# Optimization experiments

Hardware: AMD Instinct MI355X
Metric: run time of the kernel (lower is better)

Reference implementation:

```python
import jax, jax.numpy as jnp
import numpy as np

VOCAB, BLOCK, D, H, E, TOPK = 50257, 2048, 1024, 8, 8, 2
HD = D // H  # head_size = 128


def _layernorm(x, g, b, eps=1e-5):
    mu = jnp.mean(x, axis=-1, keepdims=True)
    var = jnp.mean(jnp.square(x - mu), axis=-1, keepdims=True)
    return (x - mu) * jax.lax.rsqrt(var + eps) * g + b


def setup_inputs() -> dict:
    key = jax.random.key(0)
    ks = jax.random.split(key, 12)
    s = 0.02
    return {
        "idx": jax.random.randint(ks[0], (4, BLOCK), 0, VOCAB),
        "tok_table": jax.random.normal(ks[1], (VOCAB, D), jnp.float32) * s,
        "pos_table": jax.random.normal(ks[2], (BLOCK, D), jnp.float32) * s,
        "Wq": jax.random.normal(ks[3], (H, D, HD), jnp.float32) * s,
        "Wk": jax.random.normal(ks[4], (H, D, HD), jnp.float32) * s,
        "Wv": jax.random.normal(ks[5], (H, D, HD), jnp.float32) * s,
        "Wo": jax.random.normal(ks[6], (D, D), jnp.float32) * s,
        "bo": jnp.zeros((D,), jnp.float32),
        "g1": jnp.ones((D,), jnp.float32),
        "b1": jnp.zeros((D,), jnp.float32),
        "g2": jnp.ones((D,), jnp.float32),
        "b2": jnp.zeros((D,), jnp.float32),
        "Wr": jax.random.normal(ks[7], (D, E), jnp.float32) * s,
        "br": jnp.zeros((E,), jnp.float32),
        "Wn": jax.random.normal(ks[8], (D, E), jnp.float32) * s,
        "bn": jnp.zeros((E,), jnp.float32),
    }


def reference(idx, tok_table, pos_table, Wq, Wk, Wv, Wo, bo, g1, b1, g2, b2, Wr, br, Wn, bn):
    B, T = idx.shape
    x = tok_table[idx] + pos_table[:T]  # [B,T,D]

    # --- multi-head causal self-attention (dropout off / eval mode) ---
    xn = _layernorm(x, g1, b1)
    q = jnp.einsum('btc,hcd->bhtd', xn, Wq)
    k = jnp.einsum('btc,hcd->bhtd', xn, Wk)
    v = jnp.einsum('btc,hcd->bhtd', xn, Wv)
    # NOTE: original scales by C**-0.5 where C = n_embed (not head_size)
    wei = jnp.einsum('bhtd,bhsd->bhts', q, k) * (D ** -0.5)
    causal = jnp.tril(jnp.ones((T, T), bool))
    wei = jnp.where(causal, wei, -jnp.inf)
    wei = jax.nn.softmax(wei, axis=-1)
    attn = jnp.einsum('bhts,bhsd->bhtd', wei, v)  # [B,H,T,HD]
    attn = attn.transpose(0, 2, 1, 3).reshape(B, T, D)  # concat heads
    x = x + attn @ Wo + bo  # residual

    x_norm = _layernorm(x, g2, b2)

    # --- noisy top-k router ---
    logits = x_norm @ Wr + br          # [B,T,E]
    noise_logits = x_norm @ Wn + bn    # [B,T,E]
    noise = jax.random.normal(jax.random.key(42), logits.shape, logits.dtype)
    noisy = logits + noise * jax.nn.softplus(noise_logits)
    top_vals, indices = jax.lax.top_k(noisy, TOPK)  # [B,T,K]
    probs_k = jax.nn.softmax(top_vals, axis=-1)     # softmax over -inf-scattered logits == softmax over top-k
    router_probs = jnp.sum(jax.nn.one_hot(indices, E, dtype=probs_k.dtype) * probs_k[..., None], axis=-2)

    return (x_norm, router_probs, indices, x)
```

## Files before the change

kernel.cpp:

```cpp
#include <hip/hip_runtime.h>
#include <math.h>
#include <stdint.h>

typedef __attribute__((ext_vector_type(8))) _Float16 f16x8;
typedef __attribute__((ext_vector_type(4))) _Float16 f16x4;
typedef __attribute__((ext_vector_type(4))) float f32x4;

__device__ __forceinline__ void split_f16(float x, _Float16& h, _Float16& l) {
  h = (_Float16)x;
  l = (_Float16)((x - (float)h) * 2048.0f);
}

__device__ __forceinline__ void gld16(const void* g, void* l) {
  __builtin_amdgcn_global_load_lds(
      (const __attribute__((address_space(1))) void*)g,
      (__attribute__((address_space(3))) void*)l, 16, 0, 0);
}

__device__ __forceinline__ void threefry2x32_42(uint32_t x0, uint32_t x1,
                                                uint32_t& o0, uint32_t& o1) {
  const uint32_t k0 = 0u, k1 = 42u;
  const uint32_t k2 = k0 ^ k1 ^ 0x1BD11BDAu;
  x0 += k0; x1 += k1;
#define TF_R(r) { x0 += x1; x1 = (x1 << (r)) | (x1 >> (32 - (r))); x1 ^= x0; }
  TF_R(13) TF_R(15) TF_R(26) TF_R(6)
  x0 += k1; x1 += k2 + 1u;
  TF_R(17) TF_R(29) TF_R(16) TF_R(24)
  x0 += k2; x1 += k0 + 2u;
  TF_R(13) TF_R(15) TF_R(26) TF_R(6)
  x0 += k0; x1 += k1 + 3u;
  TF_R(17) TF_R(29) TF_R(16) TF_R(24)
  x0 += k1; x1 += k2 + 4u;
  TF_R(13) TF_R(15) TF_R(26) TF_R(6)
  x0 += k2; x1 += k0 + 5u;
#undef TF_R
  o0 = x0; o1 = x1;
}

__device__ __forceinline__ float jax_erfinv_f32(float x) {
  float xx = __fmul_rn(x, x);
  float w = -log1pf(-xx);
  float p;
  if (w < 5.0f) {
    w = __fadd_rn(w, -2.5f);
    p = 2.81022636e-08f;
    p = __fadd_rn(3.43273939e-07f, __fmul_rn(p, w));
    p = __fadd_rn(-3.5233877e-06f, __fmul_rn(p, w));
    p = __fadd_rn(-4.39150654e-06f, __fmul_rn(p, w));
    p = __fadd_rn(0.00021858087f, __fmul_rn(p, w));
    p = __fadd_rn(-0.00125372503f, __fmul_rn(p, w));
    p = __fadd_rn(-0.00417768164f, __fmul_rn(p, w));
    p = __fadd_rn(0.246640727f, __fmul_rn(p, w));
    p = __fadd_rn(1.50140941f, __fmul_rn(p, w));
  } else {
    w = __fadd_rn(sqrtf(w), -3.0f);
    p = -0.000200214257f;
    p = __fadd_rn(0.000100950558f, __fmul_rn(p, w));
    p = __fadd_rn(0.00134934322f, __fmul_rn(p, w));
    p = __fadd_rn(-0.00367342844f, __fmul_rn(p, w));
    p = __fadd_rn(0.00573950773f, __fmul_rn(p, w));
    p = __fadd_rn(-0.0076224613f, __fmul_rn(p, w));
    p = __fadd_rn(0.00943887047f, __fmul_rn(p, w));
    p = __fadd_rn(1.00167406f, __fmul_rn(p, w));
    p = __fadd_rn(2.83297682f, __fmul_rn(p, w));
  }
  return __fmul_rn(p, x);
}

__device__ __forceinline__ float jax_noise(uint32_t n) {
  uint32_t o0, o1;
  threefry2x32_42(0u, n, o0, o1);
  uint32_t bits = o0 ^ o1;
  uint32_t fb = (bits >> 9) | 0x3F800000u;
  float f = __fadd_rn(__uint_as_float(fb), -1.0f);
  const float lo = __uint_as_float(0xBF7FFFFFu);
  float u = __fadd_rn(__fmul_rn(f, 2.0f), lo);
  u = fmaxf(lo, u);
  return __fmul_rn(__uint_as_float(0x3FB504F3u), jax_erfinv_f32(u));
}

__device__ __forceinline__ float block_sum_256(float v, float* buf) {
  #pragma unroll
  for (int off = 32; off > 0; off >>= 1) v += __shfl_down(v, off, 64);
  int lane = threadIdx.x & 63;
  int w = threadIdx.x >> 6;
  if (lane == 0) buf[w] = v;
  __syncthreads();
  return buf[0] + buf[1] + buf[2] + buf[3];
}

__global__ __launch_bounds__(128) void k_wsplit(
    const float* __restrict__ Wq, const float* __restrict__ Wk,
    const float* __restrict__ Wv, const float* __restrict__ Wo,
    _Float16* __restrict__ wqt_h, _Float16* __restrict__ wqt_l,
    _Float16* __restrict__ wot_h, _Float16* __restrict__ wot_l) {
  int z = blockIdx.x, tid = threadIdx.x;
  const float* src;
  int ldn, n;
  _Float16 *dh, *dl;
  if (z < 24) {
    int which = z >> 3, h = z & 7;
    src = ((which == 0) ? Wq : (which == 1) ? Wk : Wv) + (size_t)h * 1024 * 128;
    ldn = 128; n = tid;
    dh = wqt_h + (size_t)z * 128 * 1024 + (size_t)n * 1024;
    dl = wqt_l + (size_t)z * 128 * 1024 + (size_t)n * 1024;
  } else {
    int zz = z - 24;
    src = Wo; ldn = 1024; n = zz * 128 + tid;
    dh = wot_h + (size_t)n * 1024;
    dl = wot_l + (size_t)n * 1024;
  }
  for (int k0 = 0; k0 < 1024; k0 += 16) {
    f16x8 hv0, hv1, lv0, lv1;
    #pragma unroll
    for (int j = 0; j < 8; ++j) {
      _Float16 hh, ll;
      split_f16(src[(size_t)(k0 + j) * ldn + n], hh, ll);
      hv0[j] = hh; lv0[j] = ll;
    }
    #pragma unroll
    for (int j = 0; j < 8; ++j) {
      _Float16 hh, ll;
      split_f16(src[(size_t)(k0 + 8 + j) * ldn + n], hh, ll);
      hv1[j] = hh; lv1[j] = ll;
    }
    *(f16x8*)(dh + k0) = hv0; *(f16x8*)(dh + k0 + 8) = hv1;
    *(f16x8*)(dl + k0) = lv0; *(f16x8*)(dl + k0 + 8) = lv1;
  }
}

__global__ __launch_bounds__(256) void k_embed_ln1(
    const int* __restrict__ idx, const float* __restrict__ tok,
    const float* __restrict__ pos, const float* __restrict__ g1,
    const float* __restrict__ b1, float* __restrict__ x_out,
    _Float16* __restrict__ xnh, _Float16* __restrict__ xnl) {
  __shared__ float bufA[4], bufB[4];
  int r = blockIdx.x;
  int t = r & 2047;
  int token = idx[r];
  int c4 = threadIdx.x;
  float4 tv = *((const float4*)(tok + (size_t)token * 1024) + c4);
  float4 pv = *((const float4*)(pos + (size_t)t * 1024) + c4);
  float4 xv = make_float4(tv.x + pv.x, tv.y + pv.y, tv.z + pv.z, tv.w + pv.w);
  *((float4*)(x_out + (size_t)r * 1024) + c4) = xv;
  float mu = block_sum_256(xv.x + xv.y + xv.z + xv.w, bufA) * (1.0f / 1024.0f);
  float d0 = xv.x - mu, d1 = xv.y - mu, d2 = xv.z - mu, d3 = xv.w - mu;
  float var = block_sum_256(d0*d0 + d1*d1 + d2*d2 + d3*d3, bufB) * (1.0f / 1024.0f);
  float rs = rsqrtf(var + 1e-5f);
  float4 gv = *((const float4*)g1 + c4);
  float4 bv = *((const float4*)b1 + c4);
  float xn0 = d0*rs*gv.x + bv.x, xn1 = d1*rs*gv.y + bv.y;
  float xn2 = d2*rs*gv.z + bv.z, xn3 = d3*rs*gv.w + bv.w;
  f16x4 hv, lv;
  _Float16 hh, ll;
  split_f16(xn0, hh, ll); hv[0] = hh; lv[0] = ll;
  split_f16(xn1, hh, ll); hv[1] = hh; lv[1] = ll;
  split_f16(xn2, hh, ll); hv[2] = hh; lv[2] = ll;
  split_f16(xn3, hh, ll); hv[3] = hh; lv[3] = ll;
  *(f16x4*)(xnh + (size_t)r * 1024 + c4 * 4) = hv;
  *(f16x4*)(xnl + (size_t)r * 1024 + c4 * 4) = lv;
}

__global__ __launch_bounds__(256) void k_ln2(
    const float* __restrict__ x, const float* __restrict__ g2,
    const float* __restrict__ b2, float* __restrict__ xn_out) {
  __shared__ float bufA[4], bufB[4];
  int r = blockIdx.x;
  int c4 = threadIdx.x;
  float4 xv = *((const float4*)(x + (size_t)r * 1024) + c4);
  float mu = block_sum_256(xv.x + xv.y + xv.z + xv.w, bufA) * (1.0f / 1024.0f);
  float d0 = xv.x - mu, d1 = xv.y - mu, d2 = xv.z - mu, d3 = xv.w - mu;
  float var = block_sum_256(d0*d0 + d1*d1 + d2*d2 + d3*d3, bufB) * (1.0f / 1024.0f);
  float rs = rsqrtf(var + 1e-5f);
  float4 gv = *((const float4*)g2 + c4);
  float4 bv = *((const float4*)b2 + c4);
  float4 xn = make_float4(d0*rs*gv.x + bv.x, d1*rs*gv.y + bv.y,
                          d2*rs*gv.z + bv.z, d3*rs*gv.w + bv.w);
  *((float4*)(xn_out + (size_t)r * 1024) + c4) = xn;
}

__global__ __launch_bounds__(256) void k_qkv(
    const _Float16* __restrict__ xnh, const _Float16* __restrict__ xnl,
    const _Float16* __restrict__ wth, const _Float16* __restrict__ wtl,
    _Float16* __restrict__ qh, _Float16* __restrict__ ql,
    _Float16* __restrict__ kh, _Float16* __restrict__ kl,
    _Float16* __restrict__ vth, _Float16* __restrict__ vtl) {
  __shared__ __align__(16) _Float16 Ah[128 * 32], Al[128 * 32];
  __shared__ __align__(16) _Float16 Bh[128 * 32], Bl[128 * 32];
  int z = blockIdx.x;
  int which = z >> 3, h = z & 7;
  int m0 = blockIdx.y * 128;
  int tid = threadIdx.x, w = tid >> 6, lane = tid & 63;
  const _Float16* bsh = wth + (size_t)z * 128 * 1024;
  const _Float16* bsl = wtl + (size_t)z * 128 * 1024;
  f32x4 om[2][8], oc[2][8];
  const f32x4 zero4 = {0.f, 0.f, 0.f, 0.f};
  #pragma unroll
  for (int mr = 0; mr < 2; ++mr)
    #pragma unroll
    for (int nb = 0; nb < 8; ++nb) { om[mr][nb] = zero4; oc[mr][nb] = zero4; }

  for (int k0 = 0; k0 < 1024; k0 += 32) {
    __syncthreads();
    #pragma unroll
    for (int i2 = 0; i2 < 2; ++i2) {
      int r = w * 32 + i2 * 16 + (lane >> 2);
      int gs = (lane & 3) ^ ((r >> 1) & 3);
      size_t ao = (size_t)(m0 + r) * 1024 + k0 + gs * 8;
      size_t bo_ = (size_t)r * 1024 + k0 + gs * 8;
      gld16(xnh + ao, &Ah[(w * 32 + i2 * 16) * 32]);
      gld16(xnl + ao, &Al[(w * 32 + i2 * 16) * 32]);
      gld16(bsh + bo_, &Bh[(w * 32 + i2 * 16) * 32]);
      gld16(bsl + bo_, &Bl[(w * 32 + i2 * 16) * 32]);
    }
    asm volatile("s_waitcnt vmcnt(0)" ::: "memory");
    __syncthreads();
    f16x8 ah[2], al[2];
    #pragma unroll
    for (int mr = 0; mr < 2; ++mr) {
      int arow = w * 32 + mr * 16 + (lane & 15);
      int ag = (lane >> 4) ^ ((arow >> 1) & 3);
      ah[mr] = *(f16x8*)&Ah[arow * 32 + ag * 8];
      al[mr] = *(f16x8*)&Al[arow * 32 + ag * 8];
    }
    #pragma unroll
    for (int nb = 0; nb < 8; ++nb) {
      int brow = nb * 16 + (lane & 15);
      int bg = (lane >> 4) ^ ((brow >> 1) & 3);
      f16x8 b8h = *(f16x8*)&Bh[brow * 32 + bg * 8];
      f16x8 b8l = *(f16x8*)&Bl[brow * 32 + bg * 8];
      #pragma unroll
      for (int mr = 0; mr < 2; ++mr) {
        om[mr][nb] = __builtin_amdgcn_mfma_f32_16x16x32_f16(ah[mr], b8h, om[mr][nb], 0, 0, 0);
        oc[mr][nb] = __builtin_amdgcn_mfma_f32_16x16x32_f16(ah[mr], b8l, oc[mr][nb], 0, 0, 0);
        oc[mr][nb] = __builtin_amdgcn_mfma_f32_16x16x32_f16(al[mr], b8h, oc[mr][nb], 0, 0, 0);
      }
    }
  }
  int bb = m0 >> 11, tb = m0 & 2047;
  if (which < 2) {
    _Float16* OH = (which == 0) ? qh : kh;
    _Float16* OL = (which == 0) ? ql : kl;
    size_t base = (size_t)(bb * 8 + h) * 2048 * 128;
    #pragma unroll
    for (int mr = 0; mr < 2; ++mr)
      #pragma unroll
      for (int r2 = 0; r2 < 4; ++r2) {
        int t = tb + w * 32 + mr * 16 + ((lane >> 4) << 2) + r2;
        size_t roff = base + (size_t)t * 128 + (lane & 15);
        #pragma unroll
        for (int nb = 0; nb < 8; ++nb) {
          float v = om[mr][nb][r2] + oc[mr][nb][r2] * (1.0f / 2048.0f);
          _Float16 hh, ll;
          split_f16(v, hh, ll);
          OH[roff + nb * 16] = hh;
          OL[roff + nb * 16] = ll;
        }
      }
  } else {
    size_t base = (size_t)(bb * 8 + h) * 128 * 2048;
    #pragma unroll
    for (int mr = 0; mr < 2; ++mr) {
      int t4 = tb + w * 32 + mr * 16 + ((lane >> 4) << 2);
      #pragma unroll
      for (int nb = 0; nb < 8; ++nb) {
        int col = nb * 16 + (lane & 15);
        size_t off = base + (size_t)col * 2048 + t4;
        f16x4 hv, lv;
        #pragma unroll
        for (int r2 = 0; r2 < 4; ++r2) {
          _Float16 hh, ll;
          split_f16(om[mr][nb][r2] + oc[mr][nb][r2] * (1.0f / 2048.0f), hh, ll);
          hv[r2] = hh; lv[r2] = ll;
        }
        *(f16x4*)(vth + off) = hv;
        *(f16x4*)(vtl + off) = lv;
      }
    }
  }
}

__global__ __launch_bounds__(256) void k_proj_res(
    const _Float16* __restrict__ ah_, const _Float16* __restrict__ al_,
    const _Float16* __restrict__ wth, const _Float16* __restrict__ wtl,
    const float* __restrict__ bo, float* __restrict__ x_io) {
  __shared__ __align__(16) _Float16 Ah[128 * 64], Al[128 * 64];
  __shared__ __align__(16) _Float16 Bh[128 * 64], Bl[128 * 64];
  int n0 = blockIdx.x * 128;
  int m0 = blockIdx.y * 128;
  int tid = threadIdx.x, w = tid >> 6, lane = tid & 63;
  f32x4 om[2][8], oc[2][8];
  const f32x4 zero4 = {0.f, 0.f, 0.f, 0.f};
  #pragma unroll
  for (int mr = 0; mr < 2; ++mr)
    #pragma unroll
    for (int nb = 0; nb < 8; ++nb) { om[mr][nb] = zero4; oc[mr][nb] = zero4; }

  for (int k0 = 0; k0 < 1024; k0 += 64) {
    __syncthreads();
    #pragma unroll
    for (int i2 = 0; i2 < 4; ++i2) {
      int r = w * 32 + i2 * 8 + (lane >> 3);
      int gs = (lane & 7) ^ (r & 7);
      size_t ao = (size_t)(m0 + r) * 1024 + k0 + gs * 8;
      size_t bo_ = (size_t)(n0 + r) * 1024 + k0 + gs * 8;
      gld16(ah_ + ao, &Ah[(w * 32 + i2 * 8) * 64]);
      gld16(al_ + ao, &Al[(w * 32 + i2 * 8) * 64]);
      gld16(wth + bo_, &Bh[(w * 32 + i2 * 8) * 64]);
      gld16(wtl + bo_, &Bl[(w * 32 + i2 * 8) * 64]);
    }
    asm volatile("s_waitcnt vmcnt(0)" ::: "memory");
    __syncthreads();
    #pragma unroll
    for (int k2 = 0; k2 < 2; ++k2) {
      f16x8 ah[2], al[2];
      #pragma unroll
      for (int mr = 0; mr < 2; ++mr) {
        int arow = w * 32 + mr * 16 + (lane & 15);
        int ag = (k2 * 4 + (lane >> 4)) ^ (arow & 7);
        ah[mr] = *(f16x8*)&Ah[arow * 64 + ag * 8];
        al[mr] = *(f16x8*)&Al[arow * 64 + ag * 8];
      }
      #pragma unroll
      for (int nb = 0; nb < 8; ++nb) {
        int brow = nb * 16 + (lane & 15);
        int bg = (k2 * 4 + (lane >> 4)) ^ (brow & 7);
        f16x8 b8h = *(f16x8*)&Bh[brow * 64 + bg * 8];
        f16x8 b8l = *(f16x8*)&Bl[brow * 64 + bg * 8];
        #pragma unroll
        for (int mr = 0; mr < 2; ++mr) {
          om[mr][nb] = __builtin_amdgcn_mfma_f32_16x16x32_f16(ah[mr], b8h, om[mr][nb], 0, 0, 0);
          oc[mr][nb] = __builtin_amdgcn_mfma_f32_16x16x32_f16(ah[mr], b8l, oc[mr][nb], 0, 0, 0);
          oc[mr][nb] = __builtin_amdgcn_mfma_f32_16x16x32_f16(al[mr], b8h, oc[mr][nb], 0, 0, 0);
        }
      }
    }
  }
  #pragma unroll
  for (int mr = 0; mr < 2; ++mr)
    #pragma unroll
    for (int nb = 0; nb < 8; ++nb) {
      int col = n0 + nb * 16 + (lane & 15);
      float bov = bo[col];
      #pragma unroll
      for (int r2 = 0; r2 < 4; ++r2) {
        int gm = m0 + w * 32 + mr * 16 + ((lane >> 4) << 2) + r2;
        float* p = x_io + (size_t)gm * 1024 + col;
        *p += om[mr][nb][r2] + oc[mr][nb][r2] * (1.0f / 2048.0f) + bov;
      }
    }
}

__global__ __launch_bounds__(512) void k_attn(
    const _Float16* __restrict__ qhp, const _Float16* __restrict__ qlp,
    const _Float16* __restrict__ khp, const _Float16* __restrict__ klp,
    const _Float16* __restrict__ vthp, const _Float16* __restrict__ vtlp,
    _Float16* __restrict__ attn_h, _Float16* __restrict__ attn_l) {
  __shared__ __align__(16) _Float16 Ksh[2][32 * 128];
  __shared__ __align__(16) _Float16 Ksl[2][32 * 128];
  __shared__ __align__(16) _Float16 Vh[2][128 * 32];
  __shared__ __align__(16) _Float16 Vl[2][128 * 32];
  __shared__ __align__(16) _Float16 Ph8[8][16 * 32];
  __shared__ __align__(16) _Float16 Pl8[8][16 * 32];

  int bh_ = blockIdx.x;
  int b = bh_ >> 3, h = bh_ & 7;
  int qs = blockIdx.y;
  int tid = threadIdx.x;
  int w = tid >> 6, lane = tid & 63;

  size_t bh = (size_t)(b * 8 + h) * 2048 * 128;
  const _Float16* qhb = qhp + bh;
  const _Float16* qlb = qlp + bh;
  const _Float16* khb = khp + bh;
  const _Float16* klb = klp + bh;
  const _Float16* vhb = vthp + bh;
  const _Float16* vlb = vtlp + bh;
  _Float16* Ph = &Ph8[w][0];
  _Float16* Pl = &Pl8[w][0];

  const f32x4 zero4 = {0.f, 0.f, 0.f, 0.f};

  auto stage = [&](int cur, int j0) {
    int kr = (w << 2) + (lane >> 4);
    int kg = (lane & 15) ^ (kr & 7);
    size_t kgo = (size_t)(j0 + kr) * 128 + kg * 8;
    gld16(khb + kgo, &Ksh[cur][(w << 2) * 128]);
    gld16(klb + kgo, &Ksl[cur][(w << 2) * 128]);
    int vr = (w << 4) + (lane >> 2);
    int vg = (lane & 3) ^ ((vr >> 1) & 3);
    size_t vgo = (size_t)vr * 2048 + j0 + vg * 8;
    gld16(vhb + vgo, &Vh[cur][(w << 4) * 32]);
    gld16(vlb + vgo, &Vl[cur][(w << 4) * 32]);
  };

  #pragma unroll 1
  for (int pi = 0; pi < 2; ++pi) {
    int qt = pi ? (15 - qs) : qs;
    int t0 = qt << 7;
    int tW = t0 + w * 16;
    int rowBase = tW + ((lane >> 4) << 2);

    size_t qoff = (size_t)(tW + (lane & 15)) * 128 + ((lane >> 4) << 3);
    f16x8 qfh[4], qfl[4];
    #pragma unroll
    for (int kk = 0; kk < 4; ++kk) {
      qfh[kk] = *(const f16x8*)(qhb + qoff + kk * 32);
      qfl[kk] = *(const f16x8*)(qlb + qoff + kk * 32);
    }

    f32x4 om[8], oc[8];
    #pragma unroll
    for (int db = 0; db < 8; ++db) { om[db] = zero4; oc[db] = zero4; }
    float mreg[4], lreg[4];
    #pragma unroll
    for (int r2 = 0; r2 < 4; ++r2) { mreg[r2] = -INFINITY; lreg[r2] = 0.f; }

    int nt = 4 * qt + 4;
    stage(0, 0);
    asm volatile("s_waitcnt vmcnt(0)" ::: "memory");
    __syncthreads();
    int cur = 0;

    #pragma unroll 1
    for (int t = 0; t < nt; ++t) {
      if (t + 1 < nt) stage(cur ^ 1, (t + 1) * 32);
      int j0 = t * 32;

      f32x4 sm[2], sc[2];
      #pragma unroll
      for (int nb = 0; nb < 2; ++nb) { sm[nb] = zero4; sc[nb] = zero4; }
      #pragma unroll
      for (int kk = 0; kk < 4; ++kk) {
        #pragma unroll
        for (int nb = 0; nb < 2; ++nb) {
          int krow = nb * 16 + (lane & 15);
          int kg = (kk * 4 + (lane >> 4)) ^ (krow & 7);
          f16x8 kfh = *(f16x8*)&Ksh[cur][krow * 128 + kg * 8];
          f16x8 kfl = *(f16x8*)&Ksl[cur][krow * 128 + kg * 8];
          sm[nb] = __builtin_amdgcn_mfma_f32_16x16x32_f16(qfh[kk], kfh, sm[nb], 0, 0, 0);
          sc[nb] = __builtin_amdgcn_mfma_f32_16x16x32_f16(qfh[kk], kfl, sc[nb], 0, 0, 0);
          sc[nb] = __builtin_amdgcn_mfma_f32_16x16x32_f16(qfl[kk], kfh, sc[nb], 0, 0, 0);
        }
      }

      float rmax[4];
      #pragma unroll
      for (int r2 = 0; r2 < 4; ++r2) rmax[r2] = -INFINITY;
      #pragma unroll
      for (int nb = 0; nb < 2; ++nb) {
        int col = j0 + nb * 16 + (lane & 15);
        #pragma unroll
        for (int r2 = 0; r2 < 4; ++r2) {
          float sv = (sm[nb][r2] + sc[nb][r2] * (1.0f / 2048.0f)) * 0.03125f;
          sv = (col > rowBase + r2) ? -INFINITY : sv;
          sm[nb][r2] = sv;
          rmax[r2] = fmaxf(rmax[r2], sv);
        }
      }
      #pragma unroll
      for (int mk = 1; mk < 16; mk <<= 1)
        #pragma unroll
        for (int r2 = 0; r2 < 4; ++r2)
          rmax[r2] = fmaxf(rmax[r2], __shfl_xor(rmax[r2], mk, 64));
      float alpha[4], rsum[4];
      bool newmax = false;
      #pragma unroll
      for (int r2 = 0; r2 < 4; ++r2) {
        float mnew = fmaxf(mreg[r2], rmax[r2]);
        newmax |= (mnew > mreg[r2]);
        alpha[r2] = __expf(mreg[r2] - mnew);
        mreg[r2] = mnew;
        rsum[r2] = 0.f;
      }
      #pragma unroll
      for (int nb = 0; nb < 2; ++nb)
        #pragma unroll
        for (int r2 = 0; r2 < 4; ++r2) {
          float p = __expf(sm[nb][r2] - mreg[r2]);
          sm[nb][r2] = p;
          rsum[r2] += p;
        }
      #pragma unroll
      for (int mk = 1; mk < 16; mk <<= 1)
        #pragma unroll
        for (int r2 = 0; r2 < 4; ++r2)
          rsum[r2] += __shfl_xor(rsum[r2], mk, 64);
      #pragma unroll
      for (int r2 = 0; r2 < 4; ++r2)
        lreg[r2] = lreg[r2] * alpha[r2] + rsum[r2];

      #pragma unroll
      for (int nb = 0; nb < 2; ++nb) {
        int col = nb * 16 + (lane & 15);
        #pragma unroll
        for (int r2 = 0; r2 < 4; ++r2) {
          int prow = ((lane >> 4) << 2) + r2;
          int sg = (col >> 3) ^ ((prow >> 1) & 3);
          float ps = sm[nb][r2] * 16384.0f;
          _Float16 hh, ll;
          split_f16(ps, hh, ll);
          Ph[prow * 32 + sg * 8 + (col & 7)] = hh;
          Pl[prow * 32 + sg * 8 + (col & 7)] = ll;
        }
      }

      if (__any((int)newmax)) {
        #pragma unroll
        for (int db = 0; db < 8; ++db)
          #pragma unroll
          for (int r2 = 0; r2 < 4; ++r2) {
            om[db][r2] *= alpha[r2];
            oc[db][r2] *= alpha[r2];
          }
      }

      {
        int prow = lane & 15;
        int pg = (lane >> 4) ^ ((prow >> 1) & 3);
        f16x8 pah = *(f16x8*)&Ph[prow * 32 + pg * 8];
        f16x8 pal = *(f16x8*)&Pl[prow * 32 + pg * 8];
        #pragma unroll
        for (int db = 0; db < 8; ++db) {
          int vrow = db * 16 + (lane & 15);
          int vg = (lane >> 4) ^ ((vrow >> 1) & 3);
          f16x8 vfh = *(f16x8*)&Vh[cur][vrow * 32 + vg * 8];
          f16x8 vfl = *(f16x8*)&Vl[cur][vrow * 32 + vg * 8];
          om[db] = __builtin_amdgcn_mfma_f32_16x16x32_f16(pah, vfh, om[db], 0, 0, 0);
          oc[db] = __builtin_amdgcn_mfma_f32_16x16x32_f16(pah, vfl, oc[db], 0, 0, 0);
          oc[db] = __builtin_amdgcn_mfma_f32_16x16x32_f16(pal, vfh, oc[db], 0, 0, 0);
        }
      }

      asm volatile("s_waitcnt vmcnt(0)" ::: "memory");
      __syncthreads();
      cur ^= 1;
    }

    size_t obase = ((size_t)(b * 2048 + rowBase)) * 1024 + h * 128 + (lane & 15);
    #pragma unroll
    for (int r2 = 0; r2 < 4; ++r2) {
      float inv = 1.f / (lreg[r2] * 16384.0f);
      #pragma unroll
      for (int db = 0; db < 8; ++db) {
        float v = (om[db][r2] + oc[db][r2] * (1.0f / 2048.0f)) * inv;
        _Float16 hh, ll;
        split_f16(v, hh, ll);
        attn_h[obase + (size_t)r2 * 1024 + db * 16] = hh;
        attn_l[obase + (size_t)r2 * 1024 + db * 16] = ll;
      }
    }
  }
}

__global__ __launch_bounds__(256) void k_router(
    const float* __restrict__ xn, const float* __restrict__ Wr,
    const float* __restrict__ br, const float* __restrict__ Wn,
    const float* __restrict__ bn, float* __restrict__ rp_out,
    float* __restrict__ idx_out) {
  int wave = threadIdx.x >> 6, lane = threadIdx.x & 63;
  int r = blockIdx.x * 4 + wave;
  const float* xr = xn + (size_t)r * 1024;
  float acc[16];
  #pragma unroll
  for (int i = 0; i < 16; ++i) acc[i] = 0.f;
  int cbase = lane * 16;
  for (int cc = 0; cc < 16; ++cc) {
    int c = cbase + cc;
    float xv = xr[c];
    const float4* wr4 = (const float4*)(Wr + (size_t)c * 8);
    float4 w0 = wr4[0], w1 = wr4[1];
    acc[0] += xv * w0.x; acc[1] += xv * w0.y; acc[2] += xv * w0.z; acc[3] += xv * w0.w;
    acc[4] += xv * w1.x; acc[5] += xv * w1.y; acc[6] += xv * w1.z; acc[7] += xv * w1.w;
    const float4* wn4 = (const float4*)(Wn + (size_t)c * 8);
    float4 n0 = wn4[0], n1 = wn4[1];
    acc[8]  += xv * n0.x; acc[9]  += xv * n0.y; acc[10] += xv * n0.z; acc[11] += xv * n0.w;
    acc[12] += xv * n1.x; acc[13] += xv * n1.y; acc[14] += xv * n1.z; acc[15] += xv * n1.w;
  }
  #pragma unroll
  for (int i = 0; i < 16; ++i) {
    #pragma unroll
    for (int off = 32; off > 0; off >>= 1) acc[i] += __shfl_down(acc[i], off, 64);
  }
  if (lane == 0) {
    float noisy[8];
    uint32_t nbase = (uint32_t)r * 8u;
    #pragma unroll
    for (int e = 0; e < 8; ++e) {
      float lg = acc[e] + br[e];
      float x = acc[8 + e] + bn[e];
      float sp = __fadd_rn(fmaxf(x, 0.f), log1pf(expf(-fabsf(x))));
      float nz = jax_noise(nbase + (uint32_t)e);
      noisy[e] = __fadd_rn(lg, __fmul_rn(nz, sp));
    }
    float v1 = -INFINITY, v2 = -INFINITY;
    int i1 = 0, i2 = 0;
    #pragma unroll
    for (int e = 0; e < 8; ++e) {
      float vv = noisy[e];
      if (vv > v1) { v2 = v1; i2 = i1; v1 = vv; i1 = e; }
      else if (vv > v2) { v2 = vv; i2 = e; }
    }
    float e2 = expf(v2 - v1);
    float ssum = 1.f + e2;
    float p1 = 1.f / ssum, p2 = e2 / ssum;
    float rp[8];
    #pragma unroll
    for (int e = 0; e < 8; ++e) rp[e] = 0.f;
    rp[i1] = p1; rp[i2] = p2;
    float* op = rp_out + (size_t)r * 8;
    #pragma unroll
    for (int e = 0; e < 8; ++e) op[e] = rp[e];
    idx_out[(size_t)r * 2]     = (float)i1;
    idx_out[(size_t)r * 2 + 1] = (float)i2;
  }
}

extern "C" void kernel_launch(void* const* d_in, const int* in_sizes, int n_in,
                              void* d_out, int out_size, void* d_ws, size_t ws_size,
                              hipStream_t stream) {
  const int*   idx = (const int*)d_in[0];
  const float* tok = (const float*)d_in[1];
  const float* pos = (const float*)d_in[2];
  const float* Wq  = (const float*)d_in[3];
  const float* Wk  = (const float*)d_in[4];
  const float* Wv  = (const float*)d_in[5];
  const float* Wo  = (const float*)d_in[6];
  const float* bo  = (const float*)d_in[7];
  const float* g1  = (const float*)d_in[8];
  const float* b1  = (const float*)d_in[9];
  const float* g2  = (const float*)d_in[10];
  const float* b2  = (const float*)d_in[11];
  const float* Wr  = (const float*)d_in[12];
  const float* br  = (const float*)d_in[13];
  const float* Wn  = (const float*)d_in[14];
  const float* bn  = (const float*)d_in[15];

  float* out_xnorm = (float*)d_out;
  float* out_rp    = out_xnorm + 8388608;
  float* out_idx   = out_rp + 65536;
  float* out_x     = out_idx + 16384;

  _Float16* xnh  = (_Float16*)d_ws;
  _Float16* xnl  = xnh + 8388608;
  _Float16* qhp  = xnl + 8388608;
  _Float16* qlp  = qhp + 8388608;
  _Float16* khp  = qlp + 8388608;
  _Float16* klp  = khp + 8388608;
  _Float16* vthp = klp + 8388608;
  _Float16* vtlp = vthp + 8388608;
  _Float16* attn_h = xnh;
  _Float16* attn_l = xnl;
  _Float16* wqt_h = (_Float16*)out_xnorm;
  _Float16* wqt_l = wqt_h + 3145728;
  _Float16* wot_h = wqt_l + 3145728;
  _Float16* wot_l = wot_h + 1048576;

  k_wsplit<<<32, 128, 0, stream>>>(Wq, Wk, Wv, Wo, wqt_h, wqt_l, wot_h, wot_l);
  k_embed_ln1<<<8192, 256, 0, stream>>>(idx, tok, pos, g1, b1, out_x, xnh, xnl);
  k_qkv<<<dim3(24, 64), 256, 0, stream>>>(xnh, xnl, wqt_h, wqt_l,
                                          qhp, qlp, khp, klp, vthp, vtlp);
  k_attn<<<dim3(32, 8), 512, 0, stream>>>(qhp, qlp, khp, klp, vthp, vtlp,
                                          attn_h, attn_l);
  k_proj_res<<<dim3(8, 64), 256, 0, stream>>>(attn_h, attn_l, wot_h, wot_l, bo, out_x);
  k_ln2<<<8192, 256, 0, stream>>>(out_x, g2, b2, out_xnorm);
  k_router<<<2048, 256, 0, stream>>>(out_xnorm, Wr, br, Wn, bn, out_rp, out_idx);
}
```

Measured before the change: 967.5 us.

## Double-buffer LDS tiles in QKV and output-projection GEMMs to overlap loads

Converts the QKV and output-projection GEMM main loops to a two-stage LDS pipeline. The next K-slice is issued via global_load_lds into the alternate buffer before the MFMA work on the current one, and the wait sits at the end of each iteration. The aim is to hide global-memory latency behind compute. The projection kernel's K-step shrinks from 64 to 32 so shared memory stays the same size, which doubles its iteration and barrier count.

Result: no change. 958.0 us (-1.0%).

```diff
diff --git a/kernel.cpp b/kernel.cpp
--- a/kernel.cpp
+++ b/kernel.cpp
@@ -185,8 +185,8 @@
     _Float16* __restrict__ qh, _Float16* __restrict__ ql,
     _Float16* __restrict__ kh, _Float16* __restrict__ kl,
     _Float16* __restrict__ vth, _Float16* __restrict__ vtl) {
-  __shared__ __align__(16) _Float16 Ah[128 * 32], Al[128 * 32];
-  __shared__ __align__(16) _Float16 Bh[128 * 32], Bl[128 * 32];
+  __shared__ __align__(16) _Float16 Ah[2][128 * 32], Al[2][128 * 32];
+  __shared__ __align__(16) _Float16 Bh[2][128 * 32], Bl[2][128 * 32];
   int z = blockIdx.x;
   int which = z >> 3, h = z & 7;
   int m0 = blockIdx.y * 128;
@@ -200,35 +200,41 @@
     #pragma unroll
     for (int nb = 0; nb < 8; ++nb) { om[mr][nb] = zero4; oc[mr][nb] = zero4; }
 
-  for (int k0 = 0; k0 < 1024; k0 += 32) {
-    __syncthreads();
+  auto stage = [&](int cur, int k0) {
     #pragma unroll
     for (int i2 = 0; i2 < 2; ++i2) {
       int r = w * 32 + i2 * 16 + (lane >> 2);
       int gs = (lane & 3) ^ ((r >> 1) & 3);
       size_t ao = (size_t)(m0 + r) * 1024 + k0 + gs * 8;
       size_t bo_ = (size_t)r * 1024 + k0 + gs * 8;
-      gld16(xnh + ao, &Ah[(w * 32 + i2 * 16) * 32]);
-      gld16(xnl + ao, &Al[(w * 32 + i2 * 16) * 32]);
-      gld16(bsh + bo_, &Bh[(w * 32 + i2 * 16) * 32]);
-      gld16(bsl + bo_, &Bl[(w * 32 + i2 * 16) * 32]);
-    }
-    asm volatile("s_waitcnt vmcnt(0)" ::: "memory");
-    __syncthreads();
+      gld16(xnh + ao, &Ah[cur][(w * 32 + i2 * 16) * 32]);
+      gld16(xnl + ao, &Al[cur][(w * 32 + i2 * 16) * 32]);
+      gld16(bsh + bo_, &Bh[cur][(w * 32 + i2 * 16) * 32]);
+      gld16(bsl + bo_, &Bl[cur][(w * 32 + i2 * 16) * 32]);
+    }
+  };
+
+  stage(0, 0);
+  asm volatile("s_waitcnt vmcnt(0)" ::: "memory");
+  __syncthreads();
+  int cur = 0;
+
+  for (int k0 = 0; k0 < 1024; k0 += 32) {
+    if (k0 + 32 < 1024) stage(cur ^ 1, k0 + 32);
     f16x8 ah[2], al[2];
     #pragma unroll
     for (int mr = 0; mr < 2; ++mr) {
       int arow = w * 32 + mr * 16 + (lane & 15);
       int ag = (lane >> 4) ^ ((arow >> 1) & 3);
-      ah[mr] = *(f16x8*)&Ah[arow * 32 + ag * 8];
-      al[mr] = *(f16x8*)&Al[arow * 32 + ag * 8];
+      ah[mr] = *(f16x8*)&Ah[cur][arow * 32 + ag * 8];
+      al[mr] = *(f16x8*)&Al[cur][arow * 32 + ag * 8];
     }
     #pragma unroll
     for (int nb = 0; nb < 8; ++nb) {
       int brow = nb * 16 + (lane & 15);
       int bg = (lane >> 4) ^ ((brow >> 1) & 3);
-      f16x8 b8h = *(f16x8*)&Bh[brow * 32 + bg * 8];
-      f16x8 b8l = *(f16x8*)&Bl[brow * 32 + bg * 8];
+      f16x8 b8h = *(f16x8*)&Bh[cur][brow * 32 + bg * 8];
+      f16x8 b8l = *(f16x8*)&Bl[cur][brow * 32 + bg * 8];
       #pragma unroll
       for (int mr = 0; mr < 2; ++mr) {
         om[mr][nb] = __builtin_amdgcn_mfma_f32_16x16x32_f16(ah[mr], b8h, om[mr][nb], 0, 0, 0);
@@ -236,6 +242,9 @@
         oc[mr][nb] = __builtin_amdgcn_mfma_f32_16x16x32_f16(al[mr], b8h, oc[mr][nb], 0, 0, 0);
       }
     }
+    asm volatile("s_waitcnt vmcnt(0)" ::: "memory");
+    __syncthreads();
+    cur ^= 1;
   }
   int bb = m0 >> 11, tb = m0 & 2047;
   if (which < 2) {
@@ -284,8 +293,8 @@
     const _Float16* __restrict__ ah_, const _Float16* __restrict__ al_,
     const _Float16* __restrict__ wth, const _Float16* __restrict__ wtl,
     const float* __restrict__ bo, float* __restrict__ x_io) {
-  __shared__ __align__(16) _Float16 Ah[128 * 64], Al[128 * 64];
-  __shared__ __align__(16) _Float16 Bh[128 * 64], Bl[128 * 64];
+  __shared__ __align__(16) _Float16 Ah[2][128 * 32], Al[2][128 * 32];
+  __shared__ __align__(16) _Float16 Bh[2][128 * 32], Bl[2][128 * 32];
   int n0 = blockIdx.x * 128;
   int m0 = blockIdx.y * 128;
   int tid = threadIdx.x, w = tid >> 6, lane = tid & 63;
@@ -296,45 +305,51 @@
     #pragma unroll
     for (int nb = 0; nb < 8; ++nb) { om[mr][nb] = zero4; oc[mr][nb] = zero4; }
 
-  for (int k0 = 0; k0 < 1024; k0 += 64) {
-    __syncthreads();
-    #pragma unroll
-    for (int i2 = 0; i2 < 4; ++i2) {
-      int r = w * 32 + i2 * 8 + (lane >> 3);
-      int gs = (lane & 7) ^ (r & 7);
+  auto stage = [&](int cur, int k0) {
+    #pragma unroll
+    for (int i2 = 0; i2 < 2; ++i2) {
+      int r = w * 32 + i2 * 16 + (lane >> 2);
+      int gs = (lane & 3) ^ ((r >> 1) & 3);
       size_t ao = (size_t)(m0 + r) * 1024 + k0 + gs * 8;
       size_t bo_ = (size_t)(n0 + r) * 1024 + k0 + gs * 8;
-      gld16(ah_ + ao, &Ah[(w * 32 + i2 * 8) * 64]);
-      gld16(al_ + ao, &Al[(w * 32 + i2 * 8) * 64]);
-      gld16(wth + bo_, &Bh[(w * 32 + i2 * 8) * 64]);
-      gld16(wtl + bo_, &Bl[(w * 32 + i2 * 8) * 64]);
+      gld16(ah_ + ao, &Ah[cur][(w * 32 + i2 * 16) * 32]);
+      gld16(al_ + ao, &Al[cur][(w * 32 + i2 * 16) * 32]);
+      gld16(wth + bo_, &Bh[cur][(w * 32 + i2 * 16) * 32]);
+      gld16(wtl + bo_, &Bl[cur][(w * 32 + i2 * 16) * 32]);
+    }
+  };
+
+  stage(0, 0);
+  asm volatile("s_waitcnt vmcnt(0)" ::: "memory");
+  __syncthreads();
+  int cur = 0;
+
+  for (int k0 = 0; k0 < 1024; k0 += 32) {
+    if (k0 + 32 < 1024) stage(cur ^ 1, k0 + 32);
+    f16x8 ah[2], al[2];
+    #pragma unroll
+    for (int mr = 0; mr < 2; ++mr) {
+      int arow = w * 32 + mr * 16 + (lane & 15);
+      int ag = (lane >> 4) ^ ((arow >> 1) & 3);
+      ah[mr] = *(f16x8*)&Ah[cur][arow * 32 + ag * 8];
+      al[mr] = *(f16x8*)&Al[cur][arow * 32 + ag * 8];
+    }
+    #pragma unroll
+    for (int nb = 0; nb < 8; ++nb) {
+      int brow = nb * 16 + (lane & 15);
+      int bg = (lane >> 4) ^ ((brow >> 1) & 3);
+      f16x8 b8h = *(f16x8*)&Bh[cur][brow * 32 + bg * 8];
+      f16x8 b8l = *(f16x8*)&Bl[cur][brow * 32 + bg * 8];
+      #pragma unroll
+      for (int mr = 0; mr < 2; ++mr) {
+        om[mr][nb] = __builtin_amdgcn_mfma_f32_16x16x32_f16(ah[mr], b8h, om[mr][nb], 0, 0, 0);
+        oc[mr][nb] = __builtin_amdgcn_mfma_f32_16x16x32_f16(ah[mr], b8l, oc[mr][nb], 0, 0, 0);
+        oc[mr][nb] = __builtin_amdgcn_mfma_f32_16x16x32_f16(al[mr], b8h, oc[mr][nb], 0, 0, 0);
+      }
     }
     asm volatile("s_waitcnt vmcnt(0)" ::: "memory");
     __syncthreads();
-    #pragma unroll
-    for (int k2 = 0; k2 < 2; ++k2) {
-      f16x8 ah[2], al[2];
-      #pragma unroll
-      for (int mr = 0; mr < 2; ++mr) {
-        int arow = w * 32 + mr * 16 + (lane & 15);
-        int ag = (k2 * 4 + (lane >> 4)) ^ (arow & 7);
-        ah[mr] = *(f16x8*)&Ah[arow * 64 + ag * 8];
-        al[mr] = *(f16x8*)&Al[arow * 64 + ag * 8];
-      }
-      #pragma unroll
-      for (int nb = 0; nb < 8; ++nb) {
-        int brow = nb * 16 + (lane & 15);
-        int bg = (k2 * 4 + (lane >> 4)) ^ (brow & 7);
-        f16x8 b8h = *(f16x8*)&Bh[brow * 64 + bg * 8];
-        f16x8 b8l = *(f16x8*)&Bl[brow * 64 + bg * 8];
-        #pragma unroll
-        for (int mr = 0; mr < 2; ++mr) {
-          om[mr][nb] = __builtin_amdgcn_mfma_f32_16x16x32_f16(ah[mr], b8h, om[mr][nb], 0, 0, 0);
-          oc[mr][nb] = __builtin_amdgcn_mfma_f32_16x16x32_f16(ah[mr], b8l, oc[mr][nb], 0, 0, 0);
-          oc[mr][nb] = __builtin_amdgcn_mfma_f32_16x16x32_f16(al[mr], b8h, oc[mr][nb], 0, 0, 0);
-        }
-      }
-    }
+    cur ^= 1;
   }
   #pragma unroll
   for (int mr = 0; mr < 2; ++mr)
```
